# Performance work log

Measured on AMD Instinct MI355X. Metric: run time of the kernel, lower is better.

Reference implementation:

```python
import jax, jax.numpy as jnp
import numpy as np

B, D_IN, D_H, D_OUT, D_INT = 1024, 2048, 4096, 2048, 1024


def fwht(x):
    """Fast Walsh-Hadamard transform over a length-2^k vector (unnormalized),
    faithful to the torch chunk/cat butterfly loop."""
    n = x.shape[0]
    k = int(n).bit_length() - 1
    for i in range(k):
        y = x.reshape(2 ** i, 2, -1)        # split butterfly level i
        x = jnp.stack([y[:, 0] + y[:, 1], y[:, 0] - y[:, 1]], axis=1)
    return x.reshape(n)


def fastfood(V, BB, Pi, GG, DD):
    """fastfood_torched: pad -> B*x -> H -> permute -> G* -> H -> slice/scale."""
    LL = BB.shape[0]
    vpad = jnp.zeros((LL,), V.dtype).at[: V.shape[0]].set(V)
    m5 = fwht(fwht(BB * vpad)[Pi] * GG)
    divisor = jnp.sqrt(LL * jnp.sum(GG * GG))
    return m5[:DD] / (divisor * np.sqrt(float(DD) / LL))


def _ff_vars(key, DD):
    LL = 1 << int(np.ceil(np.log2(DD)))
    k1, k2, k3 = jax.random.split(key, 3)
    BB = jnp.where(jax.random.uniform(k1, (LL,)) < 0.5, -1.0, 1.0).astype(jnp.float32)
    Pi = jax.random.permutation(k2, LL).astype(jnp.int32)
    GG = jax.random.normal(k3, (LL,), dtype=jnp.float32)
    return BB, Pi, GG


def setup_inputs():
    key = jax.random.key(0)
    ks = jax.random.split(key, 8)
    x = jax.random.normal(ks[0], (B, D_IN), dtype=jnp.float32)
    V = jax.random.normal(ks[1], (D_INT,), dtype=jnp.float32) * 0.01
    W1_0 = jax.random.normal(ks[2], (D_H, D_IN), dtype=jnp.float32) * 0.02
    b1_0 = jnp.zeros((D_H,), jnp.float32)
    W2_0 = jax.random.normal(ks[3], (D_OUT, D_H), dtype=jnp.float32) * 0.02
    b2_0 = jnp.zeros((D_OUT,), jnp.float32)
    BB_W1, Pi_W1, GG_W1 = _ff_vars(ks[4], D_H * D_IN)
    BB_b1, Pi_b1, GG_b1 = _ff_vars(ks[5], D_H)
    BB_W2, Pi_W2, GG_W2 = _ff_vars(ks[6], D_OUT * D_H)
    BB_b2, Pi_b2, GG_b2 = _ff_vars(ks[7], D_OUT)
    return dict(x=x, V=V, W1_0=W1_0, b1_0=b1_0, W2_0=W2_0, b2_0=b2_0,
                BB_W1=BB_W1, Pi_W1=Pi_W1, GG_W1=GG_W1,
                BB_b1=BB_b1, Pi_b1=Pi_b1, GG_b1=GG_b1,
                BB_W2=BB_W2, Pi_W2=Pi_W2, GG_W2=GG_W2,
                BB_b2=BB_b2, Pi_b2=Pi_b2, GG_b2=GG_b2)


def reference(x, V, W1_0, b1_0, W2_0, b2_0,
              BB_W1, Pi_W1, GG_W1, BB_b1, Pi_b1, GG_b1,
              BB_W2, Pi_W2, GG_W2, BB_b2, Pi_b2, GG_b2):
    # Reconstruct each parameter: theta = theta0 + fastfood(V).view(shape)
    W1 = W1_0 + fastfood(V, BB_W1, Pi_W1, GG_W1, D_H * D_IN).reshape(D_H, D_IN)
    b1 = b1_0 + fastfood(V, BB_b1, Pi_b1, GG_b1, D_H)
    W2 = W2_0 + fastfood(V, BB_W2, Pi_W2, GG_W2, D_OUT * D_H).reshape(D_OUT, D_H)
    b2 = b2_0 + fastfood(V, BB_b2, Pi_b2, GG_b2, D_OUT)
    # Wrapped module forward (2-layer MLP)
    h = jax.nn.relu(x @ W1.T + b1)
    return h @ W2.T + b2
```

## Files before the change

kernel.cpp:

```cpp
#include <hip/hip_runtime.h>
#include <hip/hip_bf16.h>
#include <stdint.h>


typedef __attribute__((ext_vector_type(8))) short bf16x8;
typedef __attribute__((ext_vector_type(8))) short short8;
typedef __attribute__((ext_vector_type(4))) float f32x4;

__device__ __forceinline__ ushort f2bf(float f) {
  union { float f; uint32_t u; } v; v.f = f;
  return (ushort)((v.u + 0x7FFFu + ((v.u >> 16) & 1u)) >> 16);
}
__device__ __forceinline__ float bf2f(ushort u) {
  union { uint32_t u; float f; } v; v.u = (uint32_t)u << 16; return v.f;
}

__device__ __forceinline__ void gload_lds16(const void* g, void* l) {
  __builtin_amdgcn_global_load_lds(
      (const __attribute__((address_space(1))) void*)g,
      (__attribute__((address_space(3))) void*)l, 16, 0, 0);
}

__device__ __forceinline__ void wait_vm16() { asm volatile("s_waitcnt vmcnt(16)" ::: "memory"); }
__device__ __forceinline__ void wait_vm8()  { asm volatile("s_waitcnt vmcnt(8)"  ::: "memory"); }
__device__ __forceinline__ void wait_vm0()  { asm volatile("s_waitcnt vmcnt(0)"  ::: "memory"); }
__device__ __forceinline__ void wait_lgkm0(){ asm volatile("s_waitcnt lgkmcnt(0)" ::: "memory"); }
__device__ __forceinline__ void barrier_raw(){ asm volatile("s_barrier" ::: "memory"); }

template <int NN>
__device__ __forceinline__ void wht_inreg(float* v) {
#pragma unroll
  for (int h = 1; h < NN; h <<= 1)
#pragma unroll
    for (int g = 0; g < NN; g += (h << 1))
#pragma unroll
      for (int k = 0; k < h; ++k) {
        float a = v[g + k], b = v[g + k + h];
        v[g + k] = a + b; v[g + k + h] = a - b;
      }
}

__global__ __launch_bounds__(256) void make_t_kernel(
    const float* __restrict__ V, const float* __restrict__ BB1,
    const float* __restrict__ BB2, float* __restrict__ t1, float* __restrict__ t2) {
  __shared__ float ts[1024];
  const float* BB = blockIdx.x ? BB2 : BB1;
  float* t = blockIdx.x ? t2 : t1;
  int tid = threadIdx.x;
  for (int i = tid; i < 1024; i += 256) ts[i] = BB[i] * V[i];
  for (int st = 0; st < 10; ++st) {
    int half = 1 << st;
    __syncthreads();
    for (int j = tid; j < 512; j += 256) {
      int p = ((j >> st) << (st + 1)) | (j & (half - 1));
      float a = ts[p], b = ts[p + half];
      ts[p] = a + b; ts[p + half] = a - b;
    }
  }
  __syncthreads();
  for (int i = tid; i < 1024; i += 256) t[i] = ts[i];
}

__global__ __launch_bounds__(256) void make_bias_kernel(
    const float* __restrict__ V,
    const float* __restrict__ BB1, const int* __restrict__ Pi1, const float* __restrict__ GG1, const float* __restrict__ b10,
    const float* __restrict__ BB2, const int* __restrict__ Pi2, const float* __restrict__ GG2, const float* __restrict__ b20,
    float* __restrict__ ob1, float* __restrict__ ob2) {
  __shared__ float ts[1024];
  __shared__ float zs[4096];
  __shared__ float red[4];
  int tid = threadIdx.x;
  int which = blockIdx.x;
  int L = which ? 2048 : 4096;
  const float* BB = which ? BB2 : BB1;
  const int* Pi = which ? Pi2 : Pi1;
  const float* GG = which ? GG2 : GG1;
  const float* b0 = which ? b20 : b10;
  float* ob = which ? ob2 : ob1;

  for (int i = tid; i < 1024; i += 256) ts[i] = BB[i] * V[i];
  for (int st = 0; st < 10; ++st) {
    int half = 1 << st;
    __syncthreads();
    for (int j = tid; j < 512; j += 256) {
      int p = ((j >> st) << (st + 1)) | (j & (half - 1));
      float a = ts[p], b = ts[p + half];
      ts[p] = a + b; ts[p + half] = a - b;
    }
  }
  __syncthreads();
  float gsum = 0.f;
  for (int i = tid; i < L; i += 256) {
    int pi = Pi[i];
    float g = GG[i];
    gsum += g * g;
    zs[i] = ts[pi & 1023] * g;
  }
  for (int o = 32; o > 0; o >>= 1) gsum += __shfl_down(gsum, o);
  if ((tid & 63) == 0) red[tid >> 6] = gsum;
  __syncthreads();
  float ssum = red[0] + red[1] + red[2] + red[3];
  for (int st = 0; (1 << st) < L; ++st) {
    int half = 1 << st;
    __syncthreads();
    for (int j = tid; j < (L >> 1); j += 256) {
      int p = ((j >> st) << (st + 1)) | (j & (half - 1));
      float a = zs[p], b = zs[p + half];
      zs[p] = a + b; zs[p + half] = a - b;
    }
  }
  __syncthreads();
  float scale = rsqrtf((float)L * ssum);
  for (int i = tid; i < L; i += 256) ob[i] = b0[i] + zs[i] * scale;
}

__global__ __launch_bounds__(256) void ff_pass1(
    const int* __restrict__ Pi1, const float* __restrict__ GG1,
    const int* __restrict__ Pi2, const float* __restrict__ GG2,
    const float* __restrict__ t1, const float* __restrict__ t2,
    ushort* __restrict__ inter1, ushort* __restrict__ inter2,
    float* __restrict__ partials) {
  __shared__ float ts[1024];
  __shared__ float zs[8448];
  __shared__ float red[4];
  int tid = threadIdx.x;
  int wsel = blockIdx.x >> 10;
  int blk = blockIdx.x & 1023;
  const int* Pi = wsel ? Pi2 : Pi1;
  const float* GG = wsel ? GG2 : GG1;
  const float* t = wsel ? t2 : t1;
  ushort* inter = wsel ? inter2 : inter1;
  size_t base = (size_t)blk * 8192;

  for (int i = tid; i < 1024; i += 256) ts[i] = t[i];
  __syncthreads();

  const int4* Pi4 = (const int4*)(Pi + base);
  const float4* GG4 = (const float4*)(GG + base);
  float gsum = 0.f;
#pragma unroll
  for (int q = 0; q < 8; ++q) {
    int u = (q << 8) + tid;
    int4 p4 = Pi4[u];
    float4 g4 = GG4[u];
    gsum += g4.x * g4.x + g4.y * g4.y + g4.z * g4.z + g4.w * g4.w;
    int i0 = u << 2;
    float4 z;
    z.x = ts[p4.x & 1023] * g4.x;
    z.y = ts[p4.y & 1023] * g4.y;
    z.z = ts[p4.z & 1023] * g4.z;
    z.w = ts[p4.w & 1023] * g4.w;
    *(float4*)&zs[i0 + (i0 >> 5)] = z;
  }
  for (int o = 32; o > 0; o >>= 1) gsum += __shfl_down(gsum, o);
  if ((tid & 63) == 0) red[tid >> 6] = gsum;
  __syncthreads();
  if (tid == 0) partials[blockIdx.x] = red[0] + red[1] + red[2] + red[3];

  float v[32];
  {
    int o = (tid & 7) | ((tid >> 3) << 8);
#pragma unroll
    for (int r = 0; r < 32; ++r) { int i = o + (r << 3); v[r] = zs[i + (i >> 5)]; }
    wht_inreg<32>(v);
#pragma unroll
    for (int r = 0; r < 32; ++r) { int i = o + (r << 3); zs[i + (i >> 5)] = v[r]; }
  }
  __syncthreads();
  {
#pragma unroll
    for (int r = 0; r < 32; ++r) { int i = tid | (r << 8); v[r] = zs[i + (i >> 5)]; }
    wht_inreg<32>(v);
#pragma unroll
    for (int r = 0; r < 32; ++r) { int i = tid | (r << 8); zs[i + (i >> 5)] = v[r]; }
  }
  __syncthreads();
  {
    int tp = ((tid & 63) << 3) | ((tid >> 6) << 11);
#pragma unroll
    for (int j = 0; j < 4; ++j)
#pragma unroll
      for (int k = 0; k < 8; ++k) { int i = tp + (j << 9) + k; v[(j << 3) + k] = zs[i + (i >> 5)]; }
#pragma unroll
    for (int j = 0; j < 4; ++j) wht_inreg<8>(v + (j << 3));
#pragma unroll
    for (int j = 0; j < 4; ++j) {
      short8 s;
#pragma unroll
      for (int k = 0; k < 8; ++k) s[k] = (short)f2bf(v[(j << 3) + k]);
      *(short8*)(inter + base + tp + (j << 9)) = s;
    }
  }
}

__global__ __launch_bounds__(1024) void ff_pass2(
    const ushort* __restrict__ inter1, const ushort* __restrict__ inter2,
    const float* __restrict__ W01, const float* __restrict__ W02,
    const float* __restrict__ partials,
    ushort* __restrict__ W1b, ushort* __restrict__ W2b) {
  __shared__ float tile[1024 * 33];
  __shared__ float red2[16];
  int tid = threadIdx.x;
  int wsel = blockIdx.x >> 8;
  int cb = (blockIdx.x & 255) << 5;
  const ushort* inter = wsel ? inter2 : inter1;
  const float* W0 = wsel ? W02 : W01;
  ushort* Wb = wsel ? W2b : W1b;

  float s = partials[(wsel << 10) + tid];
  for (int o = 32; o > 0; o >>= 1) s += __shfl_down(s, o);
  if ((tid & 63) == 0) red2[tid >> 6] = s;
#pragma unroll
  for (int it = 0; it < 4; ++it) {
    int u = (it << 10) + tid;
    int row = u >> 2, c8 = (u & 3) << 3;
    short8 d = *(const short8*)(inter + ((size_t)row << 13) + cb + c8);
    float* tp = &tile[row * 33 + c8];
#pragma unroll
    for (int k = 0; k < 8; ++k) tp[k] = bf2f((ushort)d[k]);
  }
  __syncthreads();
  float ssum = 0.f;
#pragma unroll
  for (int k = 0; k < 16; ++k) ssum += red2[k];
  float sc = rsqrtf(8388608.f * ssum);

  float v[32];
  int c = tid & 31, g = tid >> 5;
#pragma unroll
  for (int r = 0; r < 32; ++r) v[r] = tile[((g << 5) + r) * 33 + c];
  wht_inreg<32>(v);
#pragma unroll
  for (int r = 0; r < 32; ++r) tile[((g << 5) + r) * 33 + c] = v[r];
  __syncthreads();
#pragma unroll
  for (int r = 0; r < 32; ++r) v[r] = tile[((r << 5) + g) * 33 + c];
  wht_inreg<32>(v);
#pragma unroll
  for (int r = 0; r < 32; ++r) tile[((r << 5) + g) * 33 + c] = v[r];
  __syncthreads();
#pragma unroll
  for (int it = 0; it < 4; ++it) {
    int u = (it << 10) + tid;
    int row = u >> 2, c8 = (u & 3) << 3;
    size_t gbase = ((size_t)row << 13) + cb + c8;
    const float* tp = &tile[row * 33 + c8];
    short8 o8;
#pragma unroll
    for (int k = 0; k < 8; ++k) o8[k] = (short)f2bf(tp[k] * sc + W0[gbase + k]);
    *(short8*)(Wb + gbase) = o8;
  }
}

__global__ __launch_bounds__(256) void cvt_f32_bf16(
    const float4* __restrict__ in, ushort4* __restrict__ out, int n4) {
  int i = blockIdx.x * 256 + threadIdx.x;
  if (i < n4) {
    float4 v = in[i];
    ushort4 o;
    o.x = f2bf(v.x); o.y = f2bf(v.y); o.z = f2bf(v.z); o.w = f2bf(v.w);
    out[i] = o;
  }
}

template <int EPI, int NT>
__global__ __launch_bounds__(256) void gemm_bt(
    const ushort* __restrict__ A, const ushort* __restrict__ B,
    const float* __restrict__ bias, ushort* __restrict__ Cb, float* __restrict__ Cf,
    int M, int N, int K) {
  __shared__ ushort As[4][8192];
  __shared__ ushort Bs[4][8192];
  const int tid = threadIdx.x;
  const int w = tid >> 6, l = tid & 63;
  const int wr = w >> 1, wc = w & 1;
  const int brow = blockIdx.y << 7, bcol = blockIdx.x << 7;
  const int lrow = l >> 3;
  const int csrc = ((l & 7) ^ lrow) << 3;
  const int l15 = l & 15;
  const int x7 = l15 & 7;
  const int kb = blockIdx.z * (NT << 6);
  f32x4 acc[4][4] = {};

  const ushort* pa = A + (size_t)(brow + (w << 5) + lrow) * K + kb + csrc;
  const ushort* pb = B + (size_t)(bcol + (w << 5) + lrow) * K + kb + csrc;
  const size_t K8 = (size_t)K << 3;

#define STAGE(buf, tt)                                                      \
  {                                                                         \
    const ushort* qa = pa + ((tt) << 6);                                    \
    const ushort* qb = pb + ((tt) << 6);                                    \
    _Pragma("unroll")                                                       \
    for (int i = 0; i < 4; ++i) {                                           \
      gload_lds16(qa + K8 * i, &As[buf][(((w << 2) + i) << 9)]);            \
      gload_lds16(qb + K8 * i, &Bs[buf][(((w << 2) + i) << 9)]);            \
    }                                                                       \
  }

  STAGE(0, 0); STAGE(1, 1); STAGE(2, 2);
  for (int t = 0; t < NT; ++t) {
    if (t < NT - 2) wait_vm16();
    else if (t == NT - 2) wait_vm8();
    else wait_vm0();
    barrier_raw();
    if (t + 3 < NT) STAGE((t + 3) & 3, t + 3);
    const ushort* Acur = As[t & 3];
    const ushort* Bcur = Bs[t & 3];
    bf16x8 af[2][4], bfr[2][4];
#pragma unroll
    for (int kk = 0; kk < 2; ++kk) {
      int c8 = (kk << 2) + (l >> 4);
#pragma unroll
      for (int m = 0; m < 4; ++m)
        af[kk][m] = *(const bf16x8*)&Acur[(((wr << 6) + (m << 4) + l15) << 6) + ((c8 ^ x7) << 3)];
#pragma unroll
      for (int n = 0; n < 4; ++n)
        bfr[kk][n] = *(const bf16x8*)&Bcur[(((wc << 6) + (n << 4) + l15) << 6) + ((c8 ^ x7) << 3)];
    }
    wait_lgkm0();
#pragma unroll
    for (int kk = 0; kk < 2; ++kk)
#pragma unroll
      for (int m = 0; m < 4; ++m)
#pragma unroll
        for (int n = 0; n < 4; ++n)
          acc[m][n] = __builtin_amdgcn_mfma_f32_16x16x32_bf16(af[kk][m], bfr[kk][n], acc[m][n], 0, 0, 0);
  }
#undef STAGE

  if (EPI == 0) {
#pragma unroll
    for (int n = 0; n < 4; ++n) {
      int col = bcol + (wc << 6) + (n << 4) + l15;
      float bv = bias[col];
#pragma unroll
      for (int m = 0; m < 4; ++m) {
        int row0 = brow + (wr << 6) + (m << 4) + ((l >> 4) << 2);
#pragma unroll
        for (int j = 0; j < 4; ++j) {
          float vv = fmaxf(acc[m][n][j] + bv, 0.f);
          Cb[(size_t)(row0 + j) * N + col] = f2bf(vv);
        }
      }
    }
  } else {
    float* outp = Cf + (size_t)blockIdx.z * M * N;
#pragma unroll
    for (int n = 0; n < 4; ++n) {
      int col = bcol + (wc << 6) + (n << 4) + l15;
#pragma unroll
      for (int m = 0; m < 4; ++m) {
        int row0 = brow + (wr << 6) + (m << 4) + ((l >> 4) << 2);
#pragma unroll
        for (int j = 0; j < 4; ++j)
          outp[(size_t)(row0 + j) * N + col] = acc[m][n][j];
      }
    }
  }
}

__global__ __launch_bounds__(256) void reduce_out(
    const float4* __restrict__ P, const float* __restrict__ b2,
    float4* __restrict__ out) {
  int i = blockIdx.x * 256 + threadIdx.x;
  float4 a = P[i], b = P[i + 524288];
  const float4 bb = *(const float4*)(b2 + ((i & 511) << 2));
  float4 o;
  o.x = a.x + b.x + bb.x; o.y = a.y + b.y + bb.y;
  o.z = a.z + b.z + bb.z; o.w = a.w + b.w + bb.w;
  out[i] = o;
}

extern "C" void kernel_launch(void* const* d_in, const int* in_sizes, int n_in,
                              void* d_out, int out_size, void* d_ws, size_t ws_size,
                              hipStream_t stream) {
  const float* x     = (const float*)d_in[0];
  const float* V     = (const float*)d_in[1];
  const float* W1_0  = (const float*)d_in[2];
  const float* b1_0  = (const float*)d_in[3];
  const float* W2_0  = (const float*)d_in[4];
  const float* b2_0  = (const float*)d_in[5];
  const float* BB_W1 = (const float*)d_in[6];
  const int*   Pi_W1 = (const int*)d_in[7];
  const float* GG_W1 = (const float*)d_in[8];
  const float* BB_b1 = (const float*)d_in[9];
  const int*   Pi_b1 = (const int*)d_in[10];
  const float* GG_b1 = (const float*)d_in[11];
  const float* BB_W2 = (const float*)d_in[12];
  const int*   Pi_W2 = (const int*)d_in[13];
  const float* GG_W2 = (const float*)d_in[14];
  const float* BB_b2 = (const float*)d_in[15];
  const int*   Pi_b2 = (const int*)d_in[16];
  const float* GG_b2 = (const float*)d_in[17];
  float* out = (float*)d_out;

  const size_t MB = 1048576ull;
  char* ws = (char*)d_ws;
  ushort* inter1 = (ushort*)(ws);
  float*  P      = (float*)(ws);
  ushort* inter2 = (ushort*)(ws + 16 * MB);
  ushort* W1b    = (ushort*)(ws + 32 * MB);
  ushort* W2b    = (ushort*)(ws + 48 * MB);
  ushort* xb     = (ushort*)(ws + 64 * MB);
  ushort* hb     = (ushort*)(ws + 68 * MB);
  char*   S      = ws + 76 * MB;
  float*  t1     = (float*)(S);
  float*  t2     = (float*)(S + 4096);
  float*  b1     = (float*)(S + 8192);
  float*  b2     = (float*)(S + 8192 + 16384);
  float*  parts  = (float*)(S + 8192 + 16384 + 8192);

  make_t_kernel<<<2, 256, 0, stream>>>(V, BB_W1, BB_W2, t1, t2);
  make_bias_kernel<<<2, 256, 0, stream>>>(V, BB_b1, Pi_b1, GG_b1, b1_0,
                                          BB_b2, Pi_b2, GG_b2, b2_0, b1, b2);
  cvt_f32_bf16<<<2048, 256, 0, stream>>>((const float4*)x, (ushort4*)xb, 524288);

  ff_pass1<<<2048, 256, 0, stream>>>(Pi_W1, GG_W1, Pi_W2, GG_W2, t1, t2,
                                     inter1, inter2, parts);
  ff_pass2<<<512, 1024, 0, stream>>>(inter1, inter2, W1_0, W2_0, parts, W1b, W2b);

  gemm_bt<0, 32><<<dim3(32, 8, 1), 256, 0, stream>>>(xb, W1b, b1, hb, nullptr, 1024, 4096, 2048);
  gemm_bt<1, 32><<<dim3(16, 8, 2), 256, 0, stream>>>(hb, W2b, nullptr, nullptr, P, 1024, 2048, 4096);
  reduce_out<<<2048, 256, 0, stream>>>((const float4*)P, b2, (float4*)out);
}
```

Baseline: 175.2 us.

## Restructure fastfood WHT passes: bf16 LDS staging, register-first butterfly, split second pass

ff_pass1 now processes two 8192-element chunks per 512-thread block. Each thread loads its Pi/GG entries before the barrier and does the first 32-point butterfly in registers. The LDS scratch is stored as bf16 with a padded layout, and the per-chunk gather pattern changes. The old single pass2, which staged a 1024x32 fp32 tile in LDS, is replaced by two register-only kernels that each do a strided 32-point WHT directly in global memory. This is meant to remove the large LDS footprint and its occupancy limits, at the cost of an extra global round trip of the intermediate and more bf16 rounding steps in the transform.

```diff
diff --git a/kernel.cpp b/kernel.cpp
--- a/kernel.cpp
+++ b/kernel.cpp
@@ -114,141 +114,161 @@
   for (int i = tid; i < L; i += 256) ob[i] = b0[i] + zs[i] * scale;
 }
 
-__global__ __launch_bounds__(256) void ff_pass1(
+__global__ __launch_bounds__(512) void ff_pass1(
     const int* __restrict__ Pi1, const float* __restrict__ GG1,
     const int* __restrict__ Pi2, const float* __restrict__ GG2,
     const float* __restrict__ t1, const float* __restrict__ t2,
     ushort* __restrict__ inter1, ushort* __restrict__ inter2,
     float* __restrict__ partials) {
   __shared__ float ts[1024];
-  __shared__ float zs[8448];
-  __shared__ float red[4];
-  int tid = threadIdx.x;
-  int wsel = blockIdx.x >> 10;
-  int blk = blockIdx.x & 1023;
+  __shared__ ushort zs[2][8704];
+  __shared__ float red[2][4];
+  const int tid = threadIdx.x;
+  const int half = tid >> 8;
+  const int s = tid & 255;
+  const int wsel = blockIdx.x >> 9;
+  const int chunk = ((blockIdx.x & 511) << 1) | half;
   const int* Pi = wsel ? Pi2 : Pi1;
   const float* GG = wsel ? GG2 : GG1;
   const float* t = wsel ? t2 : t1;
   ushort* inter = wsel ? inter2 : inter1;
-  size_t base = (size_t)blk * 8192;
-
-  for (int i = tid; i < 1024; i += 256) ts[i] = t[i];
-  __syncthreads();
+  const size_t base = (size_t)chunk << 13;
+  ushort* zc = zs[half];
+
+  for (int i = tid; i < 1024; i += 512) ts[i] = t[i];
 
   const int4* Pi4 = (const int4*)(Pi + base);
   const float4* GG4 = (const float4*)(GG + base);
+  int4 p4[8]; float4 g4[8];
+#pragma unroll
+  for (int j = 0; j < 8; ++j) { p4[j] = Pi4[(s << 3) + j]; g4[j] = GG4[(s << 3) + j]; }
+  __syncthreads();
+
+  float v[32];
   float gsum = 0.f;
 #pragma unroll
-  for (int q = 0; q < 8; ++q) {
-    int u = (q << 8) + tid;
-    int4 p4 = Pi4[u];
-    float4 g4 = GG4[u];
-    gsum += g4.x * g4.x + g4.y * g4.y + g4.z * g4.z + g4.w * g4.w;
-    int i0 = u << 2;
-    float4 z;
-    z.x = ts[p4.x & 1023] * g4.x;
-    z.y = ts[p4.y & 1023] * g4.y;
-    z.z = ts[p4.z & 1023] * g4.z;
-    z.w = ts[p4.w & 1023] * g4.w;
-    *(float4*)&zs[i0 + (i0 >> 5)] = z;
-  }
+  for (int j = 0; j < 8; ++j) {
+    gsum += g4[j].x * g4[j].x + g4[j].y * g4[j].y + g4[j].z * g4[j].z + g4[j].w * g4[j].w;
+    v[4 * j + 0] = ts[p4[j].x & 1023] * g4[j].x;
+    v[4 * j + 1] = ts[p4[j].y & 1023] * g4[j].y;
+    v[4 * j + 2] = ts[p4[j].z & 1023] * g4[j].z;
+    v[4 * j + 3] = ts[p4[j].w & 1023] * g4[j].w;
+  }
+  wht_inreg<32>(v);
+
   for (int o = 32; o > 0; o >>= 1) gsum += __shfl_down(gsum, o);
-  if ((tid & 63) == 0) red[tid >> 6] = gsum;
-  __syncthreads();
-  if (tid == 0) partials[blockIdx.x] = red[0] + red[1] + red[2] + red[3];
-
-  float v[32];
+  if ((s & 63) == 0) red[half][s >> 6] = gsum;
+
+#pragma unroll
+  for (int j = 0; j < 16; ++j) {
+    ushort2 u; u.x = f2bf(v[2 * j]); u.y = f2bf(v[2 * j + 1]);
+    *(ushort2*)&zc[34 * s + 2 * j] = u;
+  }
+  __syncthreads();
+  if (s == 0)
+    partials[(wsel << 10) + chunk] = red[half][0] + red[half][1] + red[half][2] + red[half][3];
+
   {
-    int o = (tid & 7) | ((tid >> 3) << 8);
-#pragma unroll
-    for (int r = 0; r < 32; ++r) { int i = o + (r << 3); v[r] = zs[i + (i >> 5)]; }
+    const int pb = (s & 31) + 1088 * (s >> 5);
+#pragma unroll
+    for (int r = 0; r < 32; ++r) v[r] = bf2f(zc[pb + 34 * r]);
     wht_inreg<32>(v);
 #pragma unroll
-    for (int r = 0; r < 32; ++r) { int i = o + (r << 3); zs[i + (i >> 5)] = v[r]; }
-  }
-  __syncthreads();
+    for (int r = 0; r < 32; ++r) zc[pb + 34 * r] = f2bf(v[r]);
+  }
+  __syncthreads();
+
   {
-#pragma unroll
-    for (int r = 0; r < 32; ++r) { int i = tid | (r << 8); v[r] = zs[i + (i >> 5)]; }
-    wht_inreg<32>(v);
-#pragma unroll
-    for (int r = 0; r < 32; ++r) { int i = tid | (r << 8); zs[i + (i >> 5)] = v[r]; }
-  }
-  __syncthreads();
-  {
-    int tp = ((tid & 63) << 3) | ((tid >> 6) << 11);
-#pragma unroll
-    for (int j = 0; j < 4; ++j)
-#pragma unroll
-      for (int k = 0; k < 8; ++k) { int i = tp + (j << 9) + k; v[(j << 3) + k] = zs[i + (i >> 5)]; }
-#pragma unroll
-    for (int j = 0; j < 4; ++j) wht_inreg<8>(v + (j << 3));
-#pragma unroll
-    for (int j = 0; j < 4; ++j) {
-      short8 s;
-#pragma unroll
-      for (int k = 0; k < 8; ++k) s[k] = (short)f2bf(v[(j << 3) + k]);
-      *(short8*)(inter + base + tp + (j << 9)) = s;
-    }
-  }
-}
-
-__global__ __launch_bounds__(1024) void ff_pass2(
+    const int pc = 4 * s + 2 * (s >> 3);
+    float w[4][8];
+#pragma unroll
+    for (int r = 0; r < 8; ++r)
+#pragma unroll
+      for (int kk = 0; kk < 2; ++kk) {
+        ushort2 u = *(const ushort2*)&zc[pc + 1088 * r + 2 * kk];
+        w[2 * kk][r] = bf2f(u.x);
+        w[2 * kk + 1][r] = bf2f(u.y);
+      }
+#pragma unroll
+    for (int k = 0; k < 4; ++k) wht_inreg<8>(w[k]);
+    ushort* op = inter + base + 4 * s;
+#pragma unroll
+    for (int r = 0; r < 8; ++r) {
+      short4 o;
+      o.x = (short)f2bf(w[0][r]); o.y = (short)f2bf(w[1][r]);
+      o.z = (short)f2bf(w[2][r]); o.w = (short)f2bf(w[3][r]);
+      *(short4*)&op[r << 10] = o;
+    }
+  }
+}
+
+__global__ __launch_bounds__(256) void ff_pass2a(
+    ushort* __restrict__ inter1, ushort* __restrict__ inter2) {
+  const int tid = threadIdx.x;
+  const int wsel = blockIdx.x >> 9;
+  const int bb = blockIdx.x & 511;
+  const int g0 = bb >> 4;
+  const int cb = (bb & 15) << 9;
+  ushort* inter = wsel ? inter2 : inter1;
+  ushort* p = inter + ((size_t)(g0 << 5) << 13) + cb + (tid << 1);
+
+  float va[32], vb[32];
+#pragma unroll
+  for (int r = 0; r < 32; ++r) {
+    ushort2 u = *(const ushort2*)(p + ((size_t)r << 13));
+    va[r] = bf2f(u.x); vb[r] = bf2f(u.y);
+  }
+  wht_inreg<32>(va);
+  wht_inreg<32>(vb);
+#pragma unroll
+  for (int r = 0; r < 32; ++r) {
+    ushort2 u; u.x = f2bf(va[r]); u.y = f2bf(vb[r]);
+    *(ushort2*)(p + ((size_t)r << 13)) = u;
+  }
+}
+
+__global__ __launch_bounds__(256) void ff_pass2b(
     const ushort* __restrict__ inter1, const ushort* __restrict__ inter2,
     const float* __restrict__ W01, const float* __restrict__ W02,
     const float* __restrict__ partials,
     ushort* __restrict__ W1b, ushort* __restrict__ W2b) {
-  __shared__ float tile[1024 * 33];
-  __shared__ float red2[16];
-  int tid = threadIdx.x;
-  int wsel = blockIdx.x >> 8;
-  int cb = (blockIdx.x & 255) << 5;
+  __shared__ float red[4];
+  const int tid = threadIdx.x;
+  const int wsel = blockIdx.x >> 9;
+  const int bb = blockIdx.x & 511;
+  const int g = bb >> 4;
+  const int cb = (bb & 15) << 9;
   const ushort* inter = wsel ? inter2 : inter1;
   const float* W0 = wsel ? W02 : W01;
   ushort* Wb = wsel ? W2b : W1b;
 
-  float s = partials[(wsel << 10) + tid];
-  for (int o = 32; o > 0; o >>= 1) s += __shfl_down(s, o);
-  if ((tid & 63) == 0) red2[tid >> 6] = s;
-#pragma unroll
-  for (int it = 0; it < 4; ++it) {
-    int u = (it << 10) + tid;
-    int row = u >> 2, c8 = (u & 3) << 3;
-    short8 d = *(const short8*)(inter + ((size_t)row << 13) + cb + c8);
-    float* tp = &tile[row * 33 + c8];
-#pragma unroll
-    for (int k = 0; k < 8; ++k) tp[k] = bf2f((ushort)d[k]);
-  }
-  __syncthreads();
   float ssum = 0.f;
 #pragma unroll
-  for (int k = 0; k < 16; ++k) ssum += red2[k];
-  float sc = rsqrtf(8388608.f * ssum);
-
-  float v[32];
-  int c = tid & 31, g = tid >> 5;
-#pragma unroll
-  for (int r = 0; r < 32; ++r) v[r] = tile[((g << 5) + r) * 33 + c];
-  wht_inreg<32>(v);
-#pragma unroll
-  for (int r = 0; r < 32; ++r) tile[((g << 5) + r) * 33 + c] = v[r];
-  __syncthreads();
-#pragma unroll
-  for (int r = 0; r < 32; ++r) v[r] = tile[((r << 5) + g) * 33 + c];
-  wht_inreg<32>(v);
-#pragma unroll
-  for (int r = 0; r < 32; ++r) tile[((r << 5) + g) * 33 + c] = v[r];
-  __syncthreads();
-#pragma unroll
-  for (int it = 0; it < 4; ++it) {
-    int u = (it << 10) + tid;
-    int row = u >> 2, c8 = (u & 3) << 3;
-    size_t gbase = ((size_t)row << 13) + cb + c8;
-    const float* tp = &tile[row * 33 + c8];
-    short8 o8;
-#pragma unroll
-    for (int k = 0; k < 8; ++k) o8[k] = (short)f2bf(tp[k] * sc + W0[gbase + k]);
-    *(short8*)(Wb + gbase) = o8;
+  for (int j = 0; j < 4; ++j) ssum += partials[(wsel << 10) + tid + (j << 8)];
+  for (int o = 32; o > 0; o >>= 1) ssum += __shfl_down(ssum, o);
+  if ((tid & 63) == 0) red[tid >> 6] = ssum;
+  __syncthreads();
+  const float sc = rsqrtf(8388608.f * (red[0] + red[1] + red[2] + red[3]));
+
+  const size_t coff = (size_t)cb + (tid << 1);
+  const ushort* p = inter + ((size_t)g << 13) + coff;
+
+  float va[32], vb[32];
+#pragma unroll
+  for (int r = 0; r < 32; ++r) {
+    ushort2 u = *(const ushort2*)(p + ((size_t)(r << 5) << 13));
+    va[r] = bf2f(u.x); vb[r] = bf2f(u.y);
+  }
+  wht_inreg<32>(va);
+  wht_inreg<32>(vb);
+#pragma unroll
+  for (int r = 0; r < 32; ++r) {
+    size_t m = (((size_t)(g + (r << 5))) << 13) + coff;
+    float2 w0 = *(const float2*)(W0 + m);
+    ushort2 u;
+    u.x = f2bf(va[r] * sc + w0.x);
+    u.y = f2bf(vb[r] * sc + w0.y);
+    *(ushort2*)(Wb + m) = u;
   }
 }
 
@@ -414,9 +434,10 @@
                                           BB_b2, Pi_b2, GG_b2, b2_0, b1, b2);
   cvt_f32_bf16<<<2048, 256, 0, stream>>>((const float4*)x, (ushort4*)xb, 524288);
 
-  ff_pass1<<<2048, 256, 0, stream>>>(Pi_W1, GG_W1, Pi_W2, GG_W2, t1, t2,
+  ff_pass1<<<1024, 512, 0, stream>>>(Pi_W1, GG_W1, Pi_W2, GG_W2, t1, t2,
                                      inter1, inter2, parts);
-  ff_pass2<<<512, 1024, 0, stream>>>(inter1, inter2, W1_0, W2_0, parts, W1b, W2b);
+  ff_pass2a<<<1024, 256, 0, stream>>>(inter1, inter2);
+  ff_pass2b<<<1024, 256, 0, stream>>>(inter1, inter2, W1_0, W2_0, parts, W1b, W2b);
 
   gemm_bt<0, 32><<<dim3(32, 8, 1), 256, 0, stream>>>(xb, W1b, b1, hb, nullptr, 1024, 4096, 2048);
   gemm_bt<1, 32><<<dim3(16, 8, 2), 256, 0, stream>>>(hb, W2b, nullptr, nullptr, P, 1024, 2048, 4096);
```

Result: slower. 181.2 us (+3.4%).

## Merge prep kernels and rework ff_pass2 with bf16 swizzled LDS tile

Applied to the files above, without the earlier changes.

Three small setup kernels (t vectors, bias fastfood, x conversion) become one launch with block-range dispatch, removing two launch gaps. ff_pass2 now processes 64-column strips with 512 threads and keeps the 1024x64 tile in LDS as bf16 with an XOR swizzle instead of a padded fp32 tile. Each thread handles two columns per WHT pass, and global loads and stores are fully vectorized. Storing intermediate WHT results in bf16 between the two passes adds rounding error, and there are fewer, larger blocks (256 in total).

```diff
diff --git a/kernel.cpp b/kernel.cpp
--- a/kernel.cpp
+++ b/kernel.cpp
@@ -40,78 +40,94 @@
       }
 }
 
-__global__ __launch_bounds__(256) void make_t_kernel(
-    const float* __restrict__ V, const float* __restrict__ BB1,
-    const float* __restrict__ BB2, float* __restrict__ t1, float* __restrict__ t2) {
-  __shared__ float ts[1024];
-  const float* BB = blockIdx.x ? BB2 : BB1;
-  float* t = blockIdx.x ? t2 : t1;
-  int tid = threadIdx.x;
-  for (int i = tid; i < 1024; i += 256) ts[i] = BB[i] * V[i];
-  for (int st = 0; st < 10; ++st) {
-    int half = 1 << st;
-    __syncthreads();
-    for (int j = tid; j < 512; j += 256) {
-      int p = ((j >> st) << (st + 1)) | (j & (half - 1));
-      float a = ts[p], b = ts[p + half];
-      ts[p] = a + b; ts[p + half] = a - b;
-    }
-  }
-  __syncthreads();
-  for (int i = tid; i < 1024; i += 256) t[i] = ts[i];
-}
-
-__global__ __launch_bounds__(256) void make_bias_kernel(
+__global__ __launch_bounds__(256) void prep(
+    const float4* __restrict__ x4, ushort4* __restrict__ xb4,
     const float* __restrict__ V,
-    const float* __restrict__ BB1, const int* __restrict__ Pi1, const float* __restrict__ GG1, const float* __restrict__ b10,
-    const float* __restrict__ BB2, const int* __restrict__ Pi2, const float* __restrict__ GG2, const float* __restrict__ b20,
+    const float* __restrict__ BBW1, const float* __restrict__ BBW2,
+    float* __restrict__ t1, float* __restrict__ t2,
+    const float* __restrict__ BBb1, const int* __restrict__ Pib1,
+    const float* __restrict__ GGb1, const float* __restrict__ b10,
+    const float* __restrict__ BBb2, const int* __restrict__ Pib2,
+    const float* __restrict__ GGb2, const float* __restrict__ b20,
     float* __restrict__ ob1, float* __restrict__ ob2) {
   __shared__ float ts[1024];
   __shared__ float zs[4096];
   __shared__ float red[4];
-  int tid = threadIdx.x;
-  int which = blockIdx.x;
-  int L = which ? 2048 : 4096;
-  const float* BB = which ? BB2 : BB1;
-  const int* Pi = which ? Pi2 : Pi1;
-  const float* GG = which ? GG2 : GG1;
-  const float* b0 = which ? b20 : b10;
-  float* ob = which ? ob2 : ob1;
-
-  for (int i = tid; i < 1024; i += 256) ts[i] = BB[i] * V[i];
-  for (int st = 0; st < 10; ++st) {
-    int half = 1 << st;
+  const int bid = blockIdx.x;
+  const int tid = threadIdx.x;
+
+  if (bid < 2048) {
+    int i = bid * 256 + tid;
+    float4 v = x4[i];
+    ushort4 o;
+    o.x = f2bf(v.x); o.y = f2bf(v.y); o.z = f2bf(v.z); o.w = f2bf(v.w);
+    xb4[i] = o;
+    return;
+  }
+
+  if (bid < 2050) {
+    const int which = bid - 2048;
+    const float* BB = which ? BBW2 : BBW1;
+    float* t = which ? t2 : t1;
+    for (int i = tid; i < 1024; i += 256) ts[i] = BB[i] * V[i];
+    for (int st = 0; st < 10; ++st) {
+      int half = 1 << st;
+      __syncthreads();
+      for (int j = tid; j < 512; j += 256) {
+        int p = ((j >> st) << (st + 1)) | (j & (half - 1));
+        float a = ts[p], b = ts[p + half];
+        ts[p] = a + b; ts[p + half] = a - b;
+      }
+    }
     __syncthreads();
-    for (int j = tid; j < 512; j += 256) {
-      int p = ((j >> st) << (st + 1)) | (j & (half - 1));
-      float a = ts[p], b = ts[p + half];
-      ts[p] = a + b; ts[p + half] = a - b;
-    }
-  }
-  __syncthreads();
-  float gsum = 0.f;
-  for (int i = tid; i < L; i += 256) {
-    int pi = Pi[i];
-    float g = GG[i];
-    gsum += g * g;
-    zs[i] = ts[pi & 1023] * g;
-  }
-  for (int o = 32; o > 0; o >>= 1) gsum += __shfl_down(gsum, o);
-  if ((tid & 63) == 0) red[tid >> 6] = gsum;
-  __syncthreads();
-  float ssum = red[0] + red[1] + red[2] + red[3];
-  for (int st = 0; (1 << st) < L; ++st) {
-    int half = 1 << st;
+    for (int i = tid; i < 1024; i += 256) t[i] = ts[i];
+    return;
+  }
+
+  {
+    const int which = bid - 2050;
+    const int L = which ? 2048 : 4096;
+    const float* BB = which ? BBb2 : BBb1;
+    const int* Pi = which ? Pib2 : Pib1;
+    const float* GG = which ? GGb2 : GGb1;
+    const float* b0 = which ? b20 : b10;
+    float* ob = which ? ob2 : ob1;
+
+    for (int i = tid; i < 1024; i += 256) ts[i] = BB[i] * V[i];
+    for (int st = 0; st < 10; ++st) {
+      int half = 1 << st;
+      __syncthreads();
+      for (int j = tid; j < 512; j += 256) {
+        int p = ((j >> st) << (st + 1)) | (j & (half - 1));
+        float a = ts[p], b = ts[p + half];
+        ts[p] = a + b; ts[p + half] = a - b;
+      }
+    }
     __syncthreads();
-    for (int j = tid; j < (L >> 1); j += 256) {
-      int p = ((j >> st) << (st + 1)) | (j & (half - 1));
-      float a = zs[p], b = zs[p + half];
-      zs[p] = a + b; zs[p + half] = a - b;
-    }
-  }
-  __syncthreads();
-  float scale = rsqrtf((float)L * ssum);
-  for (int i = tid; i < L; i += 256) ob[i] = b0[i] + zs[i] * scale;
+    float gsum = 0.f;
+    for (int i = tid; i < L; i += 256) {
+      int pi = Pi[i];
+      float g = GG[i];
+      gsum += g * g;
+      zs[i] = ts[pi & 1023] * g;
+    }
+    for (int o = 32; o > 0; o >>= 1) gsum += __shfl_down(gsum, o);
+    if ((tid & 63) == 0) red[tid >> 6] = gsum;
+    __syncthreads();
+    float ssum = red[0] + red[1] + red[2] + red[3];
+    for (int st = 0; (1 << st) < L; ++st) {
+      int half = 1 << st;
+      __syncthreads();
+      for (int j = tid; j < (L >> 1); j += 256) {
+        int p = ((j >> st) << (st + 1)) | (j & (half - 1));
+        float a = zs[p], b = zs[p + half];
+        zs[p] = a + b; zs[p + half] = a - b;
+      }
+    }
+    __syncthreads();
+    float scale = rsqrtf((float)L * ssum);
+    for (int i = tid; i < L; i += 256) ob[i] = b0[i] + zs[i] * scale;
+  }
 }
 
 __global__ __launch_bounds__(256) void ff_pass1(
@@ -193,73 +209,102 @@
   }
 }
 
-__global__ __launch_bounds__(1024) void ff_pass2(
+__global__ __launch_bounds__(512) void ff_pass2(
     const ushort* __restrict__ inter1, const ushort* __restrict__ inter2,
     const float* __restrict__ W01, const float* __restrict__ W02,
     const float* __restrict__ partials,
     ushort* __restrict__ W1b, ushort* __restrict__ W2b) {
-  __shared__ float tile[1024 * 33];
-  __shared__ float red2[16];
-  int tid = threadIdx.x;
-  int wsel = blockIdx.x >> 8;
-  int cb = (blockIdx.x & 255) << 5;
-  const ushort* inter = wsel ? inter2 : inter1;
-  const float* W0 = wsel ? W02 : W01;
-  ushort* Wb = wsel ? W2b : W1b;
-
-  float s = partials[(wsel << 10) + tid];
+  __shared__ ushort tile[65536];
+  __shared__ float red[8];
+  const int tid = threadIdx.x;
+  const int wsel = blockIdx.x >> 7;
+  const int cb = (blockIdx.x & 127) << 6;
+  const ushort* __restrict__ inter = wsel ? inter2 : inter1;
+  const float* __restrict__ W0 = wsel ? W02 : W01;
+  ushort* __restrict__ Wb = wsel ? W2b : W1b;
+  char* tb = (char*)tile;
+
+  float s = partials[(wsel << 10) + tid] + partials[(wsel << 10) + tid + 512];
   for (int o = 32; o > 0; o >>= 1) s += __shfl_down(s, o);
-  if ((tid & 63) == 0) red2[tid >> 6] = s;
-#pragma unroll
-  for (int it = 0; it < 4; ++it) {
-    int u = (it << 10) + tid;
-    int row = u >> 2, c8 = (u & 3) << 3;
-    short8 d = *(const short8*)(inter + ((size_t)row << 13) + cb + c8);
-    float* tp = &tile[row * 33 + c8];
-#pragma unroll
-    for (int k = 0; k < 8; ++k) tp[k] = bf2f((ushort)d[k]);
+  if ((tid & 63) == 0) red[tid >> 6] = s;
+
+#pragma unroll
+  for (int h = 0; h < 2; ++h) {
+    int r = tid + (h << 9);
+    const ushort* gp = inter + ((size_t)r << 13) + cb;
+#pragma unroll
+    for (int j = 0; j < 8; ++j) {
+      short8 d = *(const short8*)(gp + (j << 3));
+      *(short8*)(tb + (r << 7) + ((j ^ (r & 7)) << 4)) = d;
+    }
   }
   __syncthreads();
   float ssum = 0.f;
 #pragma unroll
-  for (int k = 0; k < 16; ++k) ssum += red2[k];
-  float sc = rsqrtf(8388608.f * ssum);
-
-  float v[32];
-  int c = tid & 31, g = tid >> 5;
-#pragma unroll
-  for (int r = 0; r < 32; ++r) v[r] = tile[((g << 5) + r) * 33 + c];
-  wht_inreg<32>(v);
-#pragma unroll
-  for (int r = 0; r < 32; ++r) tile[((g << 5) + r) * 33 + c] = v[r];
-  __syncthreads();
-#pragma unroll
-  for (int r = 0; r < 32; ++r) v[r] = tile[((r << 5) + g) * 33 + c];
-  wht_inreg<32>(v);
-#pragma unroll
-  for (int r = 0; r < 32; ++r) tile[((r << 5) + g) * 33 + c] = v[r];
-  __syncthreads();
-#pragma unroll
-  for (int it = 0; it < 4; ++it) {
-    int u = (it << 10) + tid;
-    int row = u >> 2, c8 = (u & 3) << 3;
-    size_t gbase = ((size_t)row << 13) + cb + c8;
-    const float* tp = &tile[row * 33 + c8];
-    short8 o8;
-#pragma unroll
-    for (int k = 0; k < 8; ++k) o8[k] = (short)f2bf(tp[k] * sc + W0[gbase + k]);
-    *(short8*)(Wb + gbase) = o8;
-  }
-}
-
-__global__ __launch_bounds__(256) void cvt_f32_bf16(
-    const float4* __restrict__ in, ushort4* __restrict__ out, int n4) {
-  int i = blockIdx.x * 256 + threadIdx.x;
-  if (i < n4) {
-    float4 v = in[i];
-    ushort4 o;
-    o.x = f2bf(v.x); o.y = f2bf(v.y); o.z = f2bf(v.z); o.w = f2bf(v.w);
-    out[i] = o;
+  for (int k = 0; k < 8; ++k) ssum += red[k];
+  const float sc = rsqrtf(8388608.f * ssum);
+
+  const int p = tid & 31;
+  const int j0 = p >> 2;
+  const int ob = (p & 3) << 2;
+#pragma unroll
+  for (int swp = 0; swp < 2; ++swp) {
+    const int ge = (tid >> 5) + (swp << 4);
+    float va[32], vb[32];
+#pragma unroll
+    for (int r = 0; r < 32; ++r) {
+      int row = (ge << 5) + r;
+      ushort2 u = *(const ushort2*)(tb + (row << 7) + ((j0 ^ (row & 7)) << 4) + ob);
+      va[r] = bf2f(u.x); vb[r] = bf2f(u.y);
+    }
+    wht_inreg<32>(va); wht_inreg<32>(vb);
+#pragma unroll
+    for (int r = 0; r < 32; ++r) {
+      int row = (ge << 5) + r;
+      ushort2 u; u.x = f2bf(va[r]); u.y = f2bf(vb[r]);
+      *(ushort2*)(tb + (row << 7) + ((j0 ^ (row & 7)) << 4) + ob) = u;
+    }
+  }
+  __syncthreads();
+#pragma unroll
+  for (int swp = 0; swp < 2; ++swp) {
+    const int ge = (tid >> 5) + (swp << 4);
+    float va[32], vb[32];
+#pragma unroll
+    for (int r = 0; r < 32; ++r) {
+      int row = ge + (r << 5);
+      ushort2 u = *(const ushort2*)(tb + (row << 7) + ((j0 ^ (row & 7)) << 4) + ob);
+      va[r] = bf2f(u.x); vb[r] = bf2f(u.y);
+    }
+    wht_inreg<32>(va); wht_inreg<32>(vb);
+#pragma unroll
+    for (int r = 0; r < 32; ++r) {
+      int row = ge + (r << 5);
+      ushort2 u; u.x = f2bf(va[r]); u.y = f2bf(vb[r]);
+      *(ushort2*)(tb + (row << 7) + ((j0 ^ (row & 7)) << 4) + ob) = u;
+    }
+  }
+  __syncthreads();
+#pragma unroll
+  for (int h = 0; h < 2; ++h) {
+    int r = tid + (h << 9);
+    size_t gb = ((size_t)r << 13) + cb;
+#pragma unroll
+    for (int j = 0; j < 8; ++j) {
+      short8 d = *(const short8*)(tb + (r << 7) + ((j ^ (r & 7)) << 4));
+      float4 w0a = *(const float4*)(W0 + gb + (j << 3));
+      float4 w0b = *(const float4*)(W0 + gb + (j << 3) + 4);
+      short8 o;
+      o[0] = (short)f2bf(bf2f((ushort)d[0]) * sc + w0a.x);
+      o[1] = (short)f2bf(bf2f((ushort)d[1]) * sc + w0a.y);
+      o[2] = (short)f2bf(bf2f((ushort)d[2]) * sc + w0a.z);
+      o[3] = (short)f2bf(bf2f((ushort)d[3]) * sc + w0a.w);
+      o[4] = (short)f2bf(bf2f((ushort)d[4]) * sc + w0b.x);
+      o[5] = (short)f2bf(bf2f((ushort)d[5]) * sc + w0b.y);
+      o[6] = (short)f2bf(bf2f((ushort)d[6]) * sc + w0b.z);
+      o[7] = (short)f2bf(bf2f((ushort)d[7]) * sc + w0b.w);
+      *(short8*)(Wb + gb + (j << 3)) = o;
+    }
   }
 }
 
@@ -409,14 +454,14 @@
   float*  b2     = (float*)(S + 8192 + 16384);
   float*  parts  = (float*)(S + 8192 + 16384 + 8192);
 
-  make_t_kernel<<<2, 256, 0, stream>>>(V, BB_W1, BB_W2, t1, t2);
-  make_bias_kernel<<<2, 256, 0, stream>>>(V, BB_b1, Pi_b1, GG_b1, b1_0,
-                                          BB_b2, Pi_b2, GG_b2, b2_0, b1, b2);
-  cvt_f32_bf16<<<2048, 256, 0, stream>>>((const float4*)x, (ushort4*)xb, 524288);
+  prep<<<2052, 256, 0, stream>>>((const float4*)x, (ushort4*)xb, V,
+                                 BB_W1, BB_W2, t1, t2,
+                                 BB_b1, Pi_b1, GG_b1, b1_0,
+                                 BB_b2, Pi_b2, GG_b2, b2_0, b1, b2);
 
   ff_pass1<<<2048, 256, 0, stream>>>(Pi_W1, GG_W1, Pi_W2, GG_W2, t1, t2,
                                      inter1, inter2, parts);
-  ff_pass2<<<512, 1024, 0, stream>>>(inter1, inter2, W1_0, W2_0, parts, W1b, W2b);
+  ff_pass2<<<256, 512, 0, stream>>>(inter1, inter2, W1_0, W2_0, parts, W1b, W2b);
 
   gemm_bt<0, 32><<<dim3(32, 8, 1), 256, 0, stream>>>(xb, W1b, b1, hb, nullptr, 1024, 4096, 2048);
   gemm_bt<1, 32><<<dim3(16, 8, 2), 256, 0, stream>>>(hb, W2b, nullptr, nullptr, P, 1024, 2048, 4096);
```

Result: faster. 171.5 us (-2.1%).
